# Performance work log

Measured on AMD Instinct MI355X. Metric: run time of the kernel, lower is better.

Reference implementation:

```python
import jax, jax.numpy as jnp
import numpy as np

N, DIN, DOUT = 8192, 2048, 2048


def setup_inputs() -> dict:
    key = jax.random.key(0)
    k1, k2, k3 = jax.random.split(key, 3)
    x = jax.random.normal(k1, (N, DIN), dtype=jnp.float32)
    # quantized params: uint8 kernel, uint16 bias (as produced by model.quantize)
    qkernel = jax.random.randint(k2, (DIN, DOUT), 0, 256, dtype=jnp.int32).astype(jnp.uint8)
    qbias = jax.random.randint(k3, (DOUT,), 0, 65536, dtype=jnp.int32).astype(jnp.uint16)
    scale = jnp.array(0.5, dtype=jnp.float32)
    zero_point = jnp.array(0.5, dtype=jnp.float32)
    return {"x": x, "scale": scale, "zero_point": zero_point,
            "qkernel": qkernel, "qbias": qbias}


def reference(x, scale, zero_point, qkernel, qbias) -> jnp.ndarray:
    # quantize(x, b=8, uint8): clip(round(x/scale) + zero_point, 0, 255)
    qmax = 2 ** 8 - 1
    xq = jnp.clip(jnp.round(x / scale) + zero_point, 0, qmax).astype(jnp.uint8)
    acc = jnp.dot(xq, qkernel, preferred_element_type=jnp.uint16)
    acc = (acc + qbias).astype(jnp.uint32)  # uint16 add wraps, then widen
    # dequantize: (x - zero_point) * scale  -> float32
    return (acc - zero_point) * scale
```

## Files before the change

kernel.cpp:

```cpp
#include <hip/hip_runtime.h>
#include <stdint.h>


#define NROWS 8192
#define DIN   2048
#define DOUT  2048

typedef int v4i __attribute__((ext_vector_type(4)));

__device__ inline void gload16(const uint8_t* g, uint8_t* l) {
  __builtin_amdgcn_global_load_lds(
      (__attribute__((address_space(1))) void*)(g),
      (__attribute__((address_space(3))) void*)(l), 16, 0, 0);
}

__device__ inline void wgbar() {
  __builtin_amdgcn_sched_barrier(0);
  __builtin_amdgcn_s_barrier();
  __builtin_amdgcn_sched_barrier(0);
}

__device__ inline uint32_t q4(float4 v, float inv, float z, int& sum) {
  uint32_t w = 0;
  float e[4] = {v.x, v.y, v.z, v.w};
#pragma unroll
  for (int i = 0; i < 4; ++i) {
    float tq = rintf(e[i] * inv) + z;
    tq = fminf(fmaxf(tq, 0.0f), 255.0f);
    uint32_t q = (uint32_t)tq;
    sum += (int)q;
    w |= ((q ^ 0x80u) & 0xFFu) << (8 * i);
  }
  return w;
}

__global__ __launch_bounds__(256) void kp(const float* __restrict__ x,
                                          const float* __restrict__ sp,
                                          const float* __restrict__ zpp,
                                          const void* __restrict__ qk,
                                          const void* __restrict__ qbias,
                                          uint8_t* __restrict__ xq,
                                          int* __restrict__ rs128,
                                          uint8_t* __restrict__ qkT,
                                          int* __restrict__ qb32) {
  const int t = threadIdx.x;
  if (blockIdx.x < NROWS) {
    const int row = blockIdx.x;
    const float s = sp[0], z = zpp[0];
    const float inv = 1.0f / s;
    const float4* xr = (const float4*)(x + (size_t)row * DIN);
    float4 a = xr[t];
    float4 b = xr[t + 256];
    int sum = 0;
    uint32_t w0 = q4(a, inv, z, sum);
    uint32_t w1 = q4(b, inv, z, sum);
    uint32_t* xw = (uint32_t*)(xq + (size_t)row * DIN);
    xw[t] = w0;
    xw[t + 256] = w1;
#pragma unroll
    for (int o = 32; o > 0; o >>= 1) sum += __shfl_down(sum, o);
    __shared__ int ws4[4];
    if ((t & 63) == 0) ws4[t >> 6] = sum;
    __syncthreads();
    if (t == 0) rs128[row] = 128 * (ws4[0] + ws4[1] + ws4[2] + ws4[3]);
    return;
  }
  __shared__ uint8_t tile[64][68];
  __shared__ int sflag;
  if (t == 0) sflag = 0;
  __syncthreads();
  {
    const int* q32 = (const int*)qk;
    int bad = 0;
#pragma unroll
    for (int i = 0; i < 4; ++i) bad |= ((unsigned)q32[t + 256 * i] > 255u);
    if (bad) sflag = 1;
  }
  __syncthreads();
  const int u8mode = sflag;

  const int j = blockIdx.x - NROWS;
  const int n0 = (j & 31) * 64;
  const int k0 = (j >> 5) * 64;
  const int tx = t & 15;
  const int ty = t >> 4;
  if (u8mode) {
    const uint8_t* q8 = (const uint8_t*)qk;
#pragma unroll
    for (int jj = 0; jj < 4; ++jj) {
      int r = jj * 16 + ty;
      uint32_t w = *(const uint32_t*)(q8 + (size_t)(k0 + r) * DOUT + n0 + tx * 4);
      tile[r][tx * 4 + 0] = (uint8_t)(w & 255u);
      tile[r][tx * 4 + 1] = (uint8_t)((w >> 8) & 255u);
      tile[r][tx * 4 + 2] = (uint8_t)((w >> 16) & 255u);
      tile[r][tx * 4 + 3] = (uint8_t)((w >> 24) & 255u);
    }
  } else {
    const int* q32 = (const int*)qk;
#pragma unroll
    for (int jj = 0; jj < 4; ++jj) {
      int r = jj * 16 + ty;
      int4 w = *(const int4*)(q32 + (size_t)(k0 + r) * DOUT + n0 + tx * 4);
      tile[r][tx * 4 + 0] = (uint8_t)w.x;
      tile[r][tx * 4 + 1] = (uint8_t)w.y;
      tile[r][tx * 4 + 2] = (uint8_t)w.z;
      tile[r][tx * 4 + 3] = (uint8_t)w.w;
    }
  }
  __syncthreads();
#pragma unroll
  for (int jj = 0; jj < 4; ++jj) {
    int r = jj * 16 + ty;
    uint32_t b0 = tile[tx * 4 + 0][r];
    uint32_t b1 = tile[tx * 4 + 1][r];
    uint32_t b2 = tile[tx * 4 + 2][r];
    uint32_t b3 = tile[tx * 4 + 3][r];
    *(uint32_t*)(qkT + (size_t)(n0 + r) * DIN + k0 + tx * 4) =
        (b0 ^ 0x80u) | ((b1 ^ 0x80u) << 8) | ((b2 ^ 0x80u) << 16) | ((b3 ^ 0x80u) << 24);
  }
  if (k0 == 0 && t < 64) {
    int n = n0 + t;
    qb32[n] = u8mode ? (int)((const uint16_t*)qbias)[n] : ((const int*)qbias)[n];
  }
}

__global__ __launch_bounds__(512, 2) void kg(const uint8_t* __restrict__ A,
                                             const uint8_t* __restrict__ B,
                                             const int* __restrict__ rs128,
                                             const int* __restrict__ qb32,
                                             const float* __restrict__ sp,
                                             const float* __restrict__ zpp,
                                             float* __restrict__ out) {
  __shared__ __align__(16) uint8_t lds[131072];
  const int t = threadIdx.x;
  const int l = t & 63, wid = t >> 6;
  const int wr = wid >> 2, wc = wid & 3;
  const int rl = l & 15, kgp = l >> 4;

  const int bid = blockIdx.x;
  const int swz = (bid & 7) * 32 + (bid >> 3);
  const int m0 = (swz >> 3) * 256;
  const int n0 = (swz & 7) * 256;

  const int srow = t >> 2;
  const int sc = (t & 3) ^ ((srow >> 1) & 3);
  const uint8_t* gA = A + (size_t)(m0 + srow) * DIN + sc * 16;
  const uint8_t* gA2 = gA + (size_t)128 * DIN;
  const uint8_t* gB = B + (size_t)(n0 + srow) * DIN + sc * 16;
  const uint8_t* gB2 = gB + (size_t)128 * DIN;
  const int sdst = t * 16;

#define STAGE_A(BUF, KS, KB) do {                                   \
    uint8_t* d_ = lds + (BUF) * 32768 + (KS) * 16384 + sdst;        \
    gload16(gA + (KB) + (KS) * 64, d_);                             \
    gload16(gA2 + (KB) + (KS) * 64, d_ + 8192);                     \
  } while (0)
#define STAGE_B(BUF, KS, KB) do {                                   \
    uint8_t* d_ = lds + 65536 + (BUF) * 32768 + (KS) * 16384 + sdst;\
    gload16(gB + (KB) + (KS) * 64, d_);                             \
    gload16(gB2 + (KB) + (KS) * 64, d_ + 8192);                     \
  } while (0)

  const int swl = (rl >> 1) & 3;
  const int aoff0 = (wr * 128 + rl) * 64 + ((kgp ^ swl) << 4);
  const int boff0 = 65536 + (wc * 64 + rl) * 64 + ((kgp ^ swl) << 4);

  v4i acc[8][4];
#pragma unroll
  for (int i = 0; i < 8; ++i)
#pragma unroll
    for (int j = 0; j < 4; ++j) acc[i][j] = (v4i){0, 0, 0, 0};
  v4i csum[4];
#pragma unroll
  for (int j = 0; j < 4; ++j) csum[j] = (v4i){0, 0, 0, 0};
  const v4i ones = (v4i){0x01010101, 0x01010101, 0x01010101, 0x01010101};
  v4i af[4], bf[4];

#define LD_A(MH, KH) do {                                            \
    const uint8_t* ap_ = lds + cur * 32768 + (KH) * 16384 + aoff0 + (MH) * 4096; \
    _Pragma("unroll")                                                \
    for (int q = 0; q < 4; ++q) af[q] = *(const v4i*)(ap_ + q * 1024);\
  } while (0)
#define LD_B(KH) do {                                                \
    const uint8_t* bp_ = lds + cur * 32768 + (KH) * 16384 + boff0;   \
    _Pragma("unroll")                                                \
    for (int nj = 0; nj < 4; ++nj) bf[nj] = *(const v4i*)(bp_ + nj * 1024); \
  } while (0)
#define LGKM0() do {                                                 \
    asm volatile("s_waitcnt lgkmcnt(0)" ::: "memory");               \
    __builtin_amdgcn_sched_barrier(0);                               \
  } while (0)
#define CLUSTER(MH, CS) do {                                         \
    __builtin_amdgcn_s_setprio(1);                                   \
    _Pragma("unroll")                                                \
    for (int q = 0; q < 4; ++q)                                      \
      _Pragma("unroll")                                              \
      for (int nj = 0; nj < 4; ++nj)                                 \
        acc[(MH) * 4 + q][nj] = __builtin_amdgcn_mfma_i32_16x16x64_i8(\
            af[q], bf[nj], acc[(MH) * 4 + q][nj], 0, 0, 0);          \
    if (CS) {                                                        \
      _Pragma("unroll")                                              \
      for (int nj = 0; nj < 4; ++nj)                                 \
        csum[nj] = __builtin_amdgcn_mfma_i32_16x16x64_i8(            \
            ones, bf[nj], csum[nj], 0, 0, 0);                        \
    }                                                                \
    __builtin_amdgcn_s_setprio(0);                                   \
  } while (0)

  STAGE_A(0, 0, 0);
  STAGE_B(0, 0, 0);
  STAGE_A(0, 1, 0);
  STAGE_B(0, 1, 0);
  asm volatile("s_waitcnt vmcnt(4)" ::: "memory");
  wgbar();

  int cur = 0;
  for (int tt = 0; tt < 16; ++tt) {
    const int nb = cur ^ 1;
    const int kn = ((tt + 1) & 15) * 128;

    LD_B(0);
    LD_A(0, 0);
    STAGE_A(nb, 0, kn);
    wgbar();
    LGKM0();
    CLUSTER(0, 1);
    wgbar();

    LD_A(1, 0);
    STAGE_B(nb, 0, kn);
    wgbar();
    LGKM0();
    CLUSTER(1, 0);
    asm volatile("s_waitcnt vmcnt(4)" ::: "memory");
    wgbar();

    LD_B(1);
    LD_A(0, 1);
    STAGE_A(nb, 1, kn);
    wgbar();
    LGKM0();
    CLUSTER(0, 1);
    wgbar();

    LD_A(1, 1);
    STAGE_B(nb, 1, kn);
    wgbar();
    LGKM0();
    CLUSTER(1, 0);
    asm volatile("s_waitcnt vmcnt(4)" ::: "memory");
    wgbar();

    cur = nb;
  }

  const float s = sp[0], z = zpp[0];
  int cc[4];
#pragma unroll
  for (int nj = 0; nj < 4; ++nj) cc[nj] = (csum[nj][0] << 7) + qb32[n0 + wc * 64 + nj * 16 + rl];
#pragma unroll
  for (int mi = 0; mi < 8; ++mi) {
#pragma unroll
    for (int r = 0; r < 4; ++r) {
      int row = m0 + wr * 128 + mi * 16 + kgp * 4 + r;
      int rs = rs128[row];
#pragma unroll
      for (int nj = 0; nj < 4; ++nj) {
        int col = n0 + wc * 64 + nj * 16 + rl;
        uint32_t v = (uint32_t)(acc[mi][nj][r] + rs + cc[nj]) & 0xFFFFu;
        out[(size_t)row * DOUT + col] = ((float)v - z) * s;
      }
    }
  }
#undef STAGE_A
#undef STAGE_B
#undef LD_A
#undef LD_B
#undef LGKM0
#undef CLUSTER
}

extern "C" void kernel_launch(void* const* d_in, const int* in_sizes, int n_in,
                              void* d_out, int out_size, void* d_ws, size_t ws_size,
                              hipStream_t stream) {
  const float* x   = (const float*)d_in[0];
  const float* sp  = (const float*)d_in[1];
  const float* zpp = (const float*)d_in[2];
  const void*  qk  = d_in[3];
  const void*  qb  = d_in[4];
  float* out = (float*)d_out;

  uint8_t* ws = (uint8_t*)d_ws;
  uint8_t* xq  = ws;
  uint8_t* qkT = ws + (16u << 20);
  int* rs128 = (int*)(ws + (20u << 20));
  int* qb32  = (int*)(ws + (20u << 20) + (32u << 10));

  kp<<<NROWS + (DIN / 64) * (DOUT / 64), 256, 0, stream>>>(
      x, sp, zpp, qk, qb, xq, rs128, qkT, qb32);
  kg<<<dim3(256), 512, 0, stream>>>(xq, qkT, rs128, qb32, sp, zpp, out);
}
```

Measured before the change: 162.6 us.

## Replace interleaved staging with two-tile-ahead prefetch and one barrier per step

Swaps the fine-grained schedule for a coarser double-buffered prefetch. The old loop interleaved half-tile global-to-LDS staging with MFMA clusters, using several workgroup barriers, lgkmcnt waits and setprio per K step. The new loop preloads both buffers up front, runs all four MFMA clusters of a step without barriers, then does one vmcnt(0) wait and barrier before staging the tile two steps ahead into the buffer just consumed. The aim is to cut barrier and wait overhead. The risk is that each step fully drains outstanding global loads and loses the setprio hints, so memory latency may be less well hidden.

Result: slower. 166.0 us (+2.1%).

```diff
diff --git a/kernel.cpp b/kernel.cpp
--- a/kernel.cpp
+++ b/kernel.cpp
@@ -176,22 +176,17 @@
   const v4i ones = (v4i){0x01010101, 0x01010101, 0x01010101, 0x01010101};
   v4i af[4], bf[4];
 
-#define LD_A(MH, KH) do {                                            \
-    const uint8_t* ap_ = lds + cur * 32768 + (KH) * 16384 + aoff0 + (MH) * 4096; \
+#define LD_A(BUF, MH, KH) do {                                       \
+    const uint8_t* ap_ = lds + (BUF) * 32768 + (KH) * 16384 + aoff0 + (MH) * 4096; \
     _Pragma("unroll")                                                \
     for (int q = 0; q < 4; ++q) af[q] = *(const v4i*)(ap_ + q * 1024);\
   } while (0)
-#define LD_B(KH) do {                                                \
-    const uint8_t* bp_ = lds + cur * 32768 + (KH) * 16384 + boff0;   \
+#define LD_B(BUF, KH) do {                                           \
+    const uint8_t* bp_ = lds + (BUF) * 32768 + (KH) * 16384 + boff0; \
     _Pragma("unroll")                                                \
     for (int nj = 0; nj < 4; ++nj) bf[nj] = *(const v4i*)(bp_ + nj * 1024); \
   } while (0)
-#define LGKM0() do {                                                 \
-    asm volatile("s_waitcnt lgkmcnt(0)" ::: "memory");               \
-    __builtin_amdgcn_sched_barrier(0);                               \
-  } while (0)
 #define CLUSTER(MH, CS) do {                                         \
-    __builtin_amdgcn_s_setprio(1);                                   \
     _Pragma("unroll")                                                \
     for (int q = 0; q < 4; ++q)                                      \
       _Pragma("unroll")                                              \
@@ -204,54 +199,40 @@
         csum[nj] = __builtin_amdgcn_mfma_i32_16x16x64_i8(            \
             ones, bf[nj], csum[nj], 0, 0, 0);                        \
     }                                                                \
-    __builtin_amdgcn_s_setprio(0);                                   \
   } while (0)
 
   STAGE_A(0, 0, 0);
   STAGE_B(0, 0, 0);
   STAGE_A(0, 1, 0);
   STAGE_B(0, 1, 0);
-  asm volatile("s_waitcnt vmcnt(4)" ::: "memory");
+  STAGE_A(1, 0, 128);
+  STAGE_B(1, 0, 128);
+  STAGE_A(1, 1, 128);
+  STAGE_B(1, 1, 128);
+  asm volatile("s_waitcnt vmcnt(8)" ::: "memory");
   wgbar();
 
-  int cur = 0;
   for (int tt = 0; tt < 16; ++tt) {
-    const int nb = cur ^ 1;
-    const int kn = ((tt + 1) & 15) * 128;
-
-    LD_B(0);
-    LD_A(0, 0);
-    STAGE_A(nb, 0, kn);
+    const int cur = tt & 1;
+    LD_B(cur, 0);
+    LD_A(cur, 0, 0);
+    CLUSTER(0, 1);
+    LD_A(cur, 1, 0);
+    CLUSTER(1, 0);
+    LD_B(cur, 1);
+    LD_A(cur, 0, 1);
+    CLUSTER(0, 1);
+    LD_A(cur, 1, 1);
+    CLUSTER(1, 0);
+    asm volatile("s_waitcnt vmcnt(0)" ::: "memory");
     wgbar();
-    LGKM0();
-    CLUSTER(0, 1);
-    wgbar();
-
-    LD_A(1, 0);
-    STAGE_B(nb, 0, kn);
-    wgbar();
-    LGKM0();
-    CLUSTER(1, 0);
-    asm volatile("s_waitcnt vmcnt(4)" ::: "memory");
-    wgbar();
-
-    LD_B(1);
-    LD_A(0, 1);
-    STAGE_A(nb, 1, kn);
-    wgbar();
-    LGKM0();
-    CLUSTER(0, 1);
-    wgbar();
-
-    LD_A(1, 1);
-    STAGE_B(nb, 1, kn);
-    wgbar();
-    LGKM0();
-    CLUSTER(1, 0);
-    asm volatile("s_waitcnt vmcnt(4)" ::: "memory");
-    wgbar();
-
-    cur = nb;
+    if (tt < 14) {
+      const int kn = (tt + 2) * 128;
+      STAGE_A(cur, 0, kn);
+      STAGE_B(cur, 0, kn);
+      STAGE_A(cur, 1, kn);
+      STAGE_B(cur, 1, kn);
+    }
   }
 
   const float s = sp[0], z = zpp[0];
@@ -276,7 +257,6 @@
 #undef STAGE_B
 #undef LD_A
 #undef LD_B
-#undef LGKM0
 #undef CLUSTER
 }
 
```
